# Kernel optimization log

Measured on AMD Instinct MI355X. Metric: run time of the kernel, lower is better.

Reference implementation:

```python
import jax, jax.numpy as jnp
import numpy as np

SCALE = 256 ** -0.5  # d_proj ** -0.5

def setup_inputs() -> dict:
    key = jax.random.key(0)
    k1, k2, k3, k4 = jax.random.split(key, 4)
    B, L, T = 8, 2048, 512
    Dh, Dg, Dp = 1024, 768, 256
    H = jax.random.normal(k1, (B, L, Dh), dtype=jnp.float32)
    G = jax.random.normal(k2, (B, T, Dg), dtype=jnp.float32)
    mask = jnp.zeros((B, L), dtype=jnp.int32)  # True/nonzero = masked OUT
    Wk = jax.random.normal(k3, (Dh, Dp), dtype=jnp.float32) * (Dh ** -0.5)
    Wq = jax.random.normal(k4, (Dg, Dp), dtype=jnp.float32) * (Dg ** -0.5)
    return {"H": H, "G": G, "mask": mask, "Wk": Wk, "Wq": Wq}

def reference(H, G, mask, Wk, Wq):
    # K: [B,L,Dp], Q: [B,T,Dp]
    K = jnp.einsum('bld,dp->blp', H, Wk)
    Q = jnp.einsum('btd,dp->btp', G, Wq)
    # logits over keys L: [B,T,L]
    logits = jnp.einsum('btp,blp->btl', Q, K) * SCALE
    logits = jnp.where(mask[:, None, :] != 0, -jnp.inf, logits)
    alpha = jax.nn.softmax(logits, axis=-1)  # online-softmax in torch == exact softmax
    Z = jnp.einsum('btl,bld->btd', alpha, H)  # [B,T,Dh]
    return Z
```

## Files before the change

kernel.cpp:

```cpp
#include <hip/hip_runtime.h>
#include <math.h>

#define BATCH 8
#define LKEYS 2048
#define TQ    512
#define DH    1024
#define DG    768
#define DP    256
#define SCALE 0.0625f

typedef short  short8  __attribute__((ext_vector_type(8)));
typedef float  floatx4 __attribute__((ext_vector_type(4)));
typedef unsigned short u16x4 __attribute__((ext_vector_type(4)));
typedef unsigned short u16x8 __attribute__((ext_vector_type(8)));

typedef unsigned int __attribute__((address_space(1))) as1_uint;
typedef unsigned int __attribute__((address_space(3))) as3_uint;

__device__ __forceinline__ unsigned short f2b(float f) {
    union { float f; unsigned int u; } v; v.f = f;
    unsigned int u = v.u;
    unsigned int r = u + 0x7fffu + ((u >> 16) & 1u);
    if ((u & 0x7f800000u) == 0x7f800000u) r = u;
    return (unsigned short)(r >> 16);
}

__device__ __forceinline__ void gload_lds16(const void* g, void* l) {
    __builtin_amdgcn_global_load_lds((const as1_uint*)g, (as3_uint*)l, 16, 0, 0);
}

__host__ __device__ constexpr int wcnt_vm(int vm) {
    return (vm & 15) | ((vm >> 4) << 14) | (7 << 4) | (15 << 8);
}

template<int BM, int BN, int OMODE, int SWZ>
__global__ __launch_bounds__(256) void gemm_bf16_p(
    const unsigned short* __restrict__ Ap, const unsigned short* __restrict__ Bp,
    const int* __restrict__ maskp, void* __restrict__ Cp,
    int K, int lda, int ldb, int ldc,
    long sA, long sB, long sC, long sM, float scale)
{
    constexpr int FM = BM / 32, FN = BN / 32;
    constexpr int AI = BM / 64, BI = BN / 64;
    constexpr int NL = AI + BI;

    __shared__ unsigned short As[4][BM * 32];
    __shared__ unsigned short Bs[4][BN * 32];

    int bx = blockIdx.x, by = blockIdx.y;
    if (SWZ) {
        const int gx = gridDim.x;
        const int nwg = gx * gridDim.y;
        const int f = by * gx + bx;
        const int nper = nwg >> 3;
        const int fl = (f & 7) * nper + (f >> 3);
        bx = fl % gx; by = fl / gx;
    }
    const int z    = blockIdx.z;
    const int tid  = threadIdx.x;
    const int lane = tid & 63;
    const int wid  = tid >> 6;
    const int wr   = wid >> 1, wc = wid & 1;
    const int lrow = lane & 15;
    const int g    = lane >> 4;

    const unsigned short* A = Ap + (long)z * sA + (long)(by * BM) * lda;
    const unsigned short* B = Bp + (long)z * sB + (long)(bx * BN) * ldb;
    const int srow = tid >> 2, sslot = tid & 3;

    const int nt = K / 32;
    floatx4 acc[FM][FN] = {};

    auto stage = [&](int t, int b) {
        const int k0 = t * 32;
        #pragma unroll
        for (int i = 0; i < AI; ++i)
            gload_lds16(A + (long)(srow + i * 64) * lda + k0 + sslot * 8,
                        (void*)&As[b][(i * 256 + tid) * 8]);
        #pragma unroll
        for (int i = 0; i < BI; ++i)
            gload_lds16(B + (long)(srow + i * 64) * ldb + k0 + sslot * 8,
                        (void*)&Bs[b][(i * 256 + tid) * 8]);
    };

    stage(0, 0);
    stage(1, 1);
    for (int t = 0; t < nt; ++t) {
        if (t + 2 < nt) {
            stage(t + 2, (t + 2) & 3);
            __builtin_amdgcn_s_waitcnt(wcnt_vm(2 * NL));
        } else if (t + 1 < nt) {
            __builtin_amdgcn_s_waitcnt(wcnt_vm(NL));
        } else {
            __builtin_amdgcn_s_waitcnt(wcnt_vm(0));
        }
        __builtin_amdgcn_s_barrier();
        __builtin_amdgcn_sched_barrier(0);

        const int b = t & 3;
        short8 a[FM], bf[FN];
        #pragma unroll
        for (int m = 0; m < FM; ++m)
            a[m] = *(const short8*)&As[b][(wr * (BM / 2) + m * 16 + lrow) * 32 + g * 8];
        #pragma unroll
        for (int n = 0; n < FN; ++n)
            bf[n] = *(const short8*)&Bs[b][(wc * (BN / 2) + n * 16 + lrow) * 32 + g * 8];
        __builtin_amdgcn_s_setprio(1);
        #pragma unroll
        for (int m = 0; m < FM; ++m)
            #pragma unroll
            for (int n = 0; n < FN; ++n)
                acc[m][n] = __builtin_amdgcn_mfma_f32_16x16x32_bf16(
                    a[m], bf[n], acc[m][n], 0, 0, 0);
        __builtin_amdgcn_s_setprio(0);
        __builtin_amdgcn_sched_barrier(0);
    }

    const int orow = by * BM + wr * (BM / 2);
    const int ocol = bx * BN + wc * (BN / 2);
    if (OMODE == 0) {
        float* C = (float*)Cp + (long)z * sC;
        #pragma unroll
        for (int m = 0; m < FM; ++m)
            #pragma unroll
            for (int n = 0; n < FN; ++n)
                #pragma unroll
                for (int r = 0; r < 4; ++r)
                    C[(long)(orow + m * 16 + 4 * g + r) * ldc + ocol + n * 16 + lrow]
                        = acc[m][n][r];
    } else if (OMODE == 1) {
        unsigned short* C = (unsigned short*)Cp + (long)z * sC;
        #pragma unroll
        for (int m = 0; m < FM; ++m)
            #pragma unroll
            for (int n = 0; n < FN; ++n)
                #pragma unroll
                for (int r = 0; r < 4; ++r)
                    C[(long)(orow + m * 16 + 4 * g + r) * ldc + ocol + n * 16 + lrow]
                        = f2b(acc[m][n][r]);
    } else {
        const int* mask = maskp + (long)z * sM;
        float* C = (float*)Cp + (long)z * sC;
        #pragma unroll
        for (int n = 0; n < FN; ++n) {
            int c = ocol + n * 16 + lrow;
            bool masked = (mask[c] != 0);
            #pragma unroll
            for (int m = 0; m < FM; ++m)
                #pragma unroll
                for (int r = 0; r < 4; ++r)
                    C[(long)(orow + m * 16 + 4 * g + r) * ldc + c]
                        = masked ? -INFINITY : acc[m][n][r] * scale;
        }
    }
}

template<int BM, int BN, int OMODE, int SWZ>
__global__ __launch_bounds__(256) void gemm_f32a(
    const float* __restrict__ Ap, const unsigned short* __restrict__ Bp,
    void* __restrict__ Cp, int K, int lda, int ldb, int ldc)
{
    constexpr int FM = BM / 32, FN = BN / 32;
    constexpr int AI = BM / 64, BI = BN / 64;

    __shared__ unsigned short As[2][BM * 32];
    __shared__ unsigned short Bs[2][BN * 32];

    int bx = blockIdx.x, by = blockIdx.y;
    if (SWZ) {
        const int gx = gridDim.x;
        const int nwg = gx * gridDim.y;
        const int f = by * gx + bx;
        const int nper = nwg >> 3;
        const int fl = (f & 7) * nper + (f >> 3);
        bx = fl % gx; by = fl / gx;
    }
    const int tid  = threadIdx.x;
    const int lane = tid & 63;
    const int wid  = tid >> 6;
    const int wr   = wid >> 1, wc = wid & 1;
    const int lrow = lane & 15;
    const int g    = lane >> 4;

    const float* A = Ap + (long)(by * BM) * lda;
    const unsigned short* B = Bp + (long)(bx * BN) * ldb;
    const int srow = tid >> 2, sslot = tid & 3;

    floatx4 acc[FM][FN] = {};
    const int nt = K / 32;
    int cur = 0;

    {
        float4 pa[AI][2];
        #pragma unroll
        for (int i = 0; i < AI; ++i) {
            const float* p = A + (long)(srow + i * 64) * lda + sslot * 8;
            pa[i][0] = *(const float4*)p;
            pa[i][1] = *(const float4*)(p + 4);
        }
        #pragma unroll
        for (int i = 0; i < BI; ++i)
            gload_lds16(B + (long)(srow + i * 64) * ldb + sslot * 8,
                        (void*)&Bs[0][(i * 256 + tid) * 8]);
        #pragma unroll
        for (int i = 0; i < AI; ++i) {
            u16x8 w;
            w[0] = f2b(pa[i][0].x); w[1] = f2b(pa[i][0].y);
            w[2] = f2b(pa[i][0].z); w[3] = f2b(pa[i][0].w);
            w[4] = f2b(pa[i][1].x); w[5] = f2b(pa[i][1].y);
            w[6] = f2b(pa[i][1].z); w[7] = f2b(pa[i][1].w);
            *(u16x8*)&As[0][(i * 256 + tid) * 8] = w;
        }
    }
    __syncthreads();

    for (int t = 0; t < nt; ++t) {
        float4 pa[AI][2];
        const bool pf = (t + 1 < nt);
        if (pf) {
            int k0 = (t + 1) * 32;
            #pragma unroll
            for (int i = 0; i < AI; ++i) {
                const float* p = A + (long)(srow + i * 64) * lda + k0 + sslot * 8;
                pa[i][0] = *(const float4*)p;
                pa[i][1] = *(const float4*)(p + 4);
            }
            #pragma unroll
            for (int i = 0; i < BI; ++i)
                gload_lds16(B + (long)(srow + i * 64) * ldb + k0 + sslot * 8,
                            (void*)&Bs[cur ^ 1][(i * 256 + tid) * 8]);
        }
        short8 a[FM], bf[FN];
        #pragma unroll
        for (int m = 0; m < FM; ++m)
            a[m] = *(const short8*)&As[cur][(wr * (BM / 2) + m * 16 + lrow) * 32 + g * 8];
        #pragma unroll
        for (int n = 0; n < FN; ++n)
            bf[n] = *(const short8*)&Bs[cur][(wc * (BN / 2) + n * 16 + lrow) * 32 + g * 8];
        #pragma unroll
        for (int m = 0; m < FM; ++m)
            #pragma unroll
            for (int n = 0; n < FN; ++n)
                acc[m][n] = __builtin_amdgcn_mfma_f32_16x16x32_bf16(
                    a[m], bf[n], acc[m][n], 0, 0, 0);
        if (pf) {
            #pragma unroll
            for (int i = 0; i < AI; ++i) {
                u16x8 w;
                w[0] = f2b(pa[i][0].x); w[1] = f2b(pa[i][0].y);
                w[2] = f2b(pa[i][0].z); w[3] = f2b(pa[i][0].w);
                w[4] = f2b(pa[i][1].x); w[5] = f2b(pa[i][1].y);
                w[6] = f2b(pa[i][1].z); w[7] = f2b(pa[i][1].w);
                *(u16x8*)&As[cur ^ 1][(i * 256 + tid) * 8] = w;
            }
        }
        __syncthreads();
        cur ^= 1;
    }

    const int orow = by * BM + wr * (BM / 2);
    const int ocol = bx * BN + wc * (BN / 2);
    if (OMODE == 1) {
        unsigned short* C = (unsigned short*)Cp;
        #pragma unroll
        for (int m = 0; m < FM; ++m)
            #pragma unroll
            for (int n = 0; n < FN; ++n)
                #pragma unroll
                for (int r = 0; r < 4; ++r)
                    C[(long)(orow + m * 16 + 4 * g + r) * ldc + ocol + n * 16 + lrow]
                        = f2b(acc[m][n][r]);
    } else {
        float* C = (float*)Cp;
        #pragma unroll
        for (int m = 0; m < FM; ++m)
            #pragma unroll
            for (int n = 0; n < FN; ++n)
                #pragma unroll
                for (int r = 0; r < 4; ++r)
                    C[(long)(orow + m * 16 + 4 * g + r) * ldc + ocol + n * 16 + lrow]
                        = acc[m][n][r];
    }
}

__global__ __launch_bounds__(256) void transpose_w(
    const float* __restrict__ W, unsigned short* __restrict__ WT, int D, int P)
{
    __shared__ float t[32][33];
    const int d0 = blockIdx.x * 32, p0 = blockIdx.y * 32;
    const int tx = threadIdx.x & 31, ty = threadIdx.x >> 5;
    #pragma unroll
    for (int j = 0; j < 4; ++j)
        t[ty + 8 * j][tx] = W[(long)(d0 + ty + 8 * j) * P + p0 + tx];
    __syncthreads();
    #pragma unroll
    for (int j = 0; j < 4; ++j)
        WT[(long)(p0 + ty + 8 * j) * D + d0 + tx] = f2b(t[tx][ty + 8 * j]);
}

__global__ __launch_bounds__(256) void prep_H(
    const float* __restrict__ H, unsigned short* __restrict__ Hb,
    unsigned short* __restrict__ HbT)
{
    __shared__ float tf[32][33];
    const int z = blockIdx.z;
    const int d0 = blockIdx.x * 32, l0 = blockIdx.y * 32;
    const float* Hz = H + (long)z * LKEYS * DH;
    unsigned short* Hbz = Hb + (long)z * LKEYS * DH;
    unsigned short* Tz = HbT + (long)z * DH * LKEYS;
    const int r = threadIdx.x >> 3, c = threadIdx.x & 7;
    float4 v = *(const float4*)&Hz[(long)(l0 + r) * DH + d0 + 4 * c];
    u16x4 w;
    w[0] = f2b(v.x); w[1] = f2b(v.y); w[2] = f2b(v.z); w[3] = f2b(v.w);
    *(u16x4*)&Hbz[(long)(l0 + r) * DH + d0 + 4 * c] = w;
    tf[r][4 * c + 0] = v.x; tf[r][4 * c + 1] = v.y;
    tf[r][4 * c + 2] = v.z; tf[r][4 * c + 3] = v.w;
    __syncthreads();
    u16x4 o;
    o[0] = f2b(tf[4 * c + 0][r]); o[1] = f2b(tf[4 * c + 1][r]);
    o[2] = f2b(tf[4 * c + 2][r]); o[3] = f2b(tf[4 * c + 3][r]);
    *(u16x4*)&Tz[(long)(d0 + r) * LKEYS + l0 + 4 * c] = o;
}

__global__ __launch_bounds__(256) void prep_HT(
    const float* __restrict__ H, unsigned short* __restrict__ HbT)
{
    __shared__ float tf[32][33];
    const int z = blockIdx.z;
    const int d0 = blockIdx.x * 32, l0 = blockIdx.y * 32;
    const float* Hz = H + (long)z * LKEYS * DH;
    unsigned short* Tz = HbT + (long)z * DH * LKEYS;
    const int r = threadIdx.x >> 3, c = threadIdx.x & 7;
    float4 v = *(const float4*)&Hz[(long)(l0 + r) * DH + d0 + 4 * c];
    tf[r][4 * c + 0] = v.x; tf[r][4 * c + 1] = v.y;
    tf[r][4 * c + 2] = v.z; tf[r][4 * c + 3] = v.w;
    __syncthreads();
    u16x4 o;
    o[0] = f2b(tf[4 * c + 0][r]); o[1] = f2b(tf[4 * c + 1][r]);
    o[2] = f2b(tf[4 * c + 2][r]); o[3] = f2b(tf[4 * c + 3][r]);
    *(u16x4*)&Tz[(long)(d0 + r) * LKEYS + l0 + 4 * c] = o;
}

__global__ __launch_bounds__(256) void prep_G(
    const float* __restrict__ G, unsigned short* __restrict__ Gb)
{
    long i = ((long)blockIdx.x * 256 + threadIdx.x) * 8;
    float4 a = *(const float4*)&G[i];
    float4 b = *(const float4*)&G[i + 4];
    u16x8 w;
    w[0] = f2b(a.x); w[1] = f2b(a.y); w[2] = f2b(a.z); w[3] = f2b(a.w);
    w[4] = f2b(b.x); w[5] = f2b(b.y); w[6] = f2b(b.z); w[7] = f2b(b.w);
    *(u16x8*)&Gb[i] = w;
}

__global__ __launch_bounds__(256) void softmax_kernel(
    const float* __restrict__ S, unsigned short* __restrict__ Ab)
{
    const float4* row4 = (const float4*)(S + (long)blockIdx.x * LKEYS);
    u16x4* out4 = (u16x4*)(Ab + (long)blockIdx.x * LKEYS);
    const int tid = threadIdx.x;
    __shared__ float red[4];

    float4 v0 = row4[tid], v1 = row4[tid + 256];
    float m = fmaxf(fmaxf(fmaxf(v0.x, v0.y), fmaxf(v0.z, v0.w)),
                    fmaxf(fmaxf(v1.x, v1.y), fmaxf(v1.z, v1.w)));
    #pragma unroll
    for (int off = 32; off > 0; off >>= 1) m = fmaxf(m, __shfl_xor(m, off));
    if ((tid & 63) == 0) red[tid >> 6] = m;
    __syncthreads();
    m = fmaxf(fmaxf(red[0], red[1]), fmaxf(red[2], red[3]));

    float e[8];
    e[0] = __expf(v0.x - m); e[1] = __expf(v0.y - m);
    e[2] = __expf(v0.z - m); e[3] = __expf(v0.w - m);
    e[4] = __expf(v1.x - m); e[5] = __expf(v1.y - m);
    e[6] = __expf(v1.z - m); e[7] = __expf(v1.w - m);
    float s = ((e[0] + e[1]) + (e[2] + e[3])) + ((e[4] + e[5]) + (e[6] + e[7]));
    #pragma unroll
    for (int off = 32; off > 0; off >>= 1) s += __shfl_xor(s, off);
    __syncthreads();
    if ((tid & 63) == 0) red[tid >> 6] = s;
    __syncthreads();
    s = red[0] + red[1] + red[2] + red[3];

    float inv = 1.0f / s;
    u16x4 a0, a1;
    a0[0] = f2b(e[0] * inv); a0[1] = f2b(e[1] * inv);
    a0[2] = f2b(e[2] * inv); a0[3] = f2b(e[3] * inv);
    a1[0] = f2b(e[4] * inv); a1[1] = f2b(e[5] * inv);
    a1[2] = f2b(e[6] * inv); a1[3] = f2b(e[7] * inv);
    out4[tid] = a0; out4[tid + 256] = a1;
}

extern "C" void kernel_launch(void* const* d_in, const int* in_sizes, int n_in,
                              void* d_out, int out_size, void* d_ws, size_t ws_size,
                              hipStream_t stream)
{
    const float* H    = (const float*)d_in[0];
    const float* G    = (const float*)d_in[1];
    const int*   mask = (const int*)  d_in[2];
    const float* Wk   = (const float*)d_in[3];
    const float* Wq   = (const float*)d_in[4];
    float*       Z    = (float*)d_out;

    unsigned short* WkT = (unsigned short*)d_ws;
    unsigned short* WqT = WkT + 262144;
    unsigned short* Ab  = WqT + 196608;

    transpose_w<<<dim3(DH / 32, DP / 32), 256, 0, stream>>>(Wk, WkT, DH, DP);
    transpose_w<<<dim3(DG / 32, DP / 32), 256, 0, stream>>>(Wq, WqT, DG, DP);

    const size_t NEED_A = 101580800ull;

    if (ws_size >= NEED_A) {
        unsigned short* Kb  = Ab  + 8388608;
        unsigned short* Qb  = Kb  + 4194304;
        unsigned short* Gb  = Qb  + 1048576;
        unsigned short* HbT = Gb  + 3145728;
        unsigned short* Hb  = HbT + 16777216;
        float*          S   = (float*)Hb;

        prep_G<<<1536, 256, 0, stream>>>(G, Gb);
        prep_H<<<dim3(DH / 32, LKEYS / 32, BATCH), 256, 0, stream>>>(H, Hb, HbT);

        gemm_bf16_p<128, 64, 1, 1><<<dim3(4, 128, 1), 256, 0, stream>>>(
            Hb, WkT, nullptr, Kb, DH, DH, DH, DP, 0, 0, 0, 0, 1.f);

        gemm_bf16_p<64, 64, 1, 1><<<dim3(4, 64, 1), 256, 0, stream>>>(
            Gb, WqT, nullptr, Qb, DG, DG, DG, DP, 0, 0, 0, 0, 1.f);

        gemm_bf16_p<128, 64, 2, 0><<<dim3(32, 4, BATCH), 256, 0, stream>>>(
            Qb, Kb, mask, S, DP, DP, DP, LKEYS,
            (long)TQ * DP, (long)LKEYS * DP, (long)TQ * LKEYS, (long)LKEYS, SCALE);

        softmax_kernel<<<BATCH * TQ, 256, 0, stream>>>(S, Ab);

        gemm_bf16_p<128, 64, 0, 1><<<dim3(16, 4, BATCH), 256, 0, stream>>>(
            Ab, HbT, nullptr, Z, LKEYS, LKEYS, LKEYS, DH,
            (long)TQ * LKEYS, (long)DH * LKEYS, (long)TQ * DH, 0, 1.f);
    } else {
        unsigned short* R   = Ab + 8388608;
        unsigned short* Kb  = R;
        unsigned short* Qb  = Kb + 4194304;
        float*          S   = (float*)(Qb + 1048576);
        unsigned short* HbT = R;

        gemm_f32a<128, 64, 1, 1><<<dim3(4, 128, 1), 256, 0, stream>>>(
            H, WkT, Kb, DH, DH, DH, DP);
        gemm_f32a<64, 64, 1, 1><<<dim3(4, 64, 1), 256, 0, stream>>>(
            G, WqT, Qb, DG, DG, DG, DP);

        gemm_bf16_p<128, 64, 2, 0><<<dim3(32, 4, BATCH), 256, 0, stream>>>(
            Qb, Kb, mask, S, DP, DP, DP, LKEYS,
            (long)TQ * DP, (long)LKEYS * DP, (long)TQ * LKEYS, (long)LKEYS, SCALE);

        softmax_kernel<<<BATCH * TQ, 256, 0, stream>>>(S, Ab);

        prep_HT<<<dim3(DH / 32, LKEYS / 32, BATCH), 256, 0, stream>>>(H, HbT);

        gemm_bf16_p<128, 64, 0, 1><<<dim3(16, 4, BATCH), 256, 0, stream>>>(
            Ab, HbT, nullptr, Z, LKEYS, LKEYS, LKEYS, DH,
            (long)TQ * LKEYS, (long)DH * LKEYS, (long)TQ * DH, 0, 1.f);
    }
}
```

Baseline: 126.4 us.

## Split-K the final attention GEMM, deepen LDS prefetch, drop fallback path

The final alpha·H GEMM is split along the key dimension into two halves. This doubles the grid from 512 to 1024 workgroups, and a reduce_add kernel then sums the two fp32 partial outputs into Z. The GEMM pipeline now prefetches three stages ahead instead of two, with each stage issued after the barrier. The QK^T logits GEMM now uses block swizzling, the low-workspace fallback path is removed, and the vmcnt encoding drops its high bits. The split costs an extra 32 MB partial-output write plus a read-back and an extra kernel launch, and it assumes the workspace is always large enough.

```diff
diff --git a/kernel.cpp b/kernel.cpp
--- a/kernel.cpp
+++ b/kernel.cpp
@@ -30,15 +30,15 @@
 }
 
 __host__ __device__ constexpr int wcnt_vm(int vm) {
-    return (vm & 15) | ((vm >> 4) << 14) | (7 << 4) | (15 << 8);
-}
-
-template<int BM, int BN, int OMODE, int SWZ>
+    return (vm & 15) | (7 << 4) | (15 << 8);
+}
+
+template<int BM, int BN, int OMODE, int SWZ, int KSPLIT>
 __global__ __launch_bounds__(256) void gemm_bf16_p(
     const unsigned short* __restrict__ Ap, const unsigned short* __restrict__ Bp,
     const int* __restrict__ maskp, void* __restrict__ Cp,
     int K, int lda, int ldb, int ldc,
-    long sA, long sB, long sC, long sM, float scale)
+    long sA, long sB, long sC, long sM, long sP, float scale)
 {
     constexpr int FM = BM / 32, FN = BN / 32;
     constexpr int AI = BM / 64, BI = BN / 64;
@@ -56,7 +56,11 @@
         const int fl = (f & 7) * nper + (f >> 3);
         bx = fl % gx; by = fl / gx;
     }
-    const int z    = blockIdx.z;
+    const int zz   = blockIdx.z;
+    const int z    = (KSPLIT == 2) ? (zz & 7) : zz;
+    const int half = (KSPLIT == 2) ? (zz >> 3) : 0;
+    const int koff = half * K;
+
     const int tid  = threadIdx.x;
     const int lane = tid & 63;
     const int wid  = tid >> 6;
@@ -64,8 +68,8 @@
     const int lrow = lane & 15;
     const int g    = lane >> 4;
 
-    const unsigned short* A = Ap + (long)z * sA + (long)(by * BM) * lda;
-    const unsigned short* B = Bp + (long)z * sB + (long)(bx * BN) * ldb;
+    const unsigned short* A = Ap + (long)z * sA + (long)(by * BM) * lda + koff;
+    const unsigned short* B = Bp + (long)z * sB + (long)(bx * BN) * ldb + koff;
     const int srow = tid >> 2, sslot = tid & 3;
 
     const int nt = K / 32;
@@ -85,16 +89,14 @@
 
     stage(0, 0);
     stage(1, 1);
+    stage(2, 2);
     for (int t = 0; t < nt; ++t) {
-        if (t + 2 < nt) {
-            stage(t + 2, (t + 2) & 3);
-            __builtin_amdgcn_s_waitcnt(wcnt_vm(2 * NL));
-        } else if (t + 1 < nt) {
-            __builtin_amdgcn_s_waitcnt(wcnt_vm(NL));
-        } else {
-            __builtin_amdgcn_s_waitcnt(wcnt_vm(0));
-        }
+        if (t < nt - 2)      __builtin_amdgcn_s_waitcnt(wcnt_vm(2 * NL));
+        else if (t == nt - 2) __builtin_amdgcn_s_waitcnt(wcnt_vm(NL));
+        else                  __builtin_amdgcn_s_waitcnt(wcnt_vm(0));
         __builtin_amdgcn_s_barrier();
+        __builtin_amdgcn_sched_barrier(0);
+        if (t + 3 < nt) stage(t + 3, (t + 3) & 3);
         __builtin_amdgcn_sched_barrier(0);
 
         const int b = t & 3;
@@ -119,7 +121,7 @@
     const int orow = by * BM + wr * (BM / 2);
     const int ocol = bx * BN + wc * (BN / 2);
     if (OMODE == 0) {
-        float* C = (float*)Cp + (long)z * sC;
+        float* C = (float*)Cp + (long)z * sC + (long)half * sP;
         #pragma unroll
         for (int m = 0; m < FM; ++m)
             #pragma unroll
@@ -155,132 +157,13 @@
     }
 }
 
-template<int BM, int BN, int OMODE, int SWZ>
-__global__ __launch_bounds__(256) void gemm_f32a(
-    const float* __restrict__ Ap, const unsigned short* __restrict__ Bp,
-    void* __restrict__ Cp, int K, int lda, int ldb, int ldc)
-{
-    constexpr int FM = BM / 32, FN = BN / 32;
-    constexpr int AI = BM / 64, BI = BN / 64;
-
-    __shared__ unsigned short As[2][BM * 32];
-    __shared__ unsigned short Bs[2][BN * 32];
-
-    int bx = blockIdx.x, by = blockIdx.y;
-    if (SWZ) {
-        const int gx = gridDim.x;
-        const int nwg = gx * gridDim.y;
-        const int f = by * gx + bx;
-        const int nper = nwg >> 3;
-        const int fl = (f & 7) * nper + (f >> 3);
-        bx = fl % gx; by = fl / gx;
-    }
-    const int tid  = threadIdx.x;
-    const int lane = tid & 63;
-    const int wid  = tid >> 6;
-    const int wr   = wid >> 1, wc = wid & 1;
-    const int lrow = lane & 15;
-    const int g    = lane >> 4;
-
-    const float* A = Ap + (long)(by * BM) * lda;
-    const unsigned short* B = Bp + (long)(bx * BN) * ldb;
-    const int srow = tid >> 2, sslot = tid & 3;
-
-    floatx4 acc[FM][FN] = {};
-    const int nt = K / 32;
-    int cur = 0;
-
-    {
-        float4 pa[AI][2];
-        #pragma unroll
-        for (int i = 0; i < AI; ++i) {
-            const float* p = A + (long)(srow + i * 64) * lda + sslot * 8;
-            pa[i][0] = *(const float4*)p;
-            pa[i][1] = *(const float4*)(p + 4);
-        }
-        #pragma unroll
-        for (int i = 0; i < BI; ++i)
-            gload_lds16(B + (long)(srow + i * 64) * ldb + sslot * 8,
-                        (void*)&Bs[0][(i * 256 + tid) * 8]);
-        #pragma unroll
-        for (int i = 0; i < AI; ++i) {
-            u16x8 w;
-            w[0] = f2b(pa[i][0].x); w[1] = f2b(pa[i][0].y);
-            w[2] = f2b(pa[i][0].z); w[3] = f2b(pa[i][0].w);
-            w[4] = f2b(pa[i][1].x); w[5] = f2b(pa[i][1].y);
-            w[6] = f2b(pa[i][1].z); w[7] = f2b(pa[i][1].w);
-            *(u16x8*)&As[0][(i * 256 + tid) * 8] = w;
-        }
-    }
-    __syncthreads();
-
-    for (int t = 0; t < nt; ++t) {
-        float4 pa[AI][2];
-        const bool pf = (t + 1 < nt);
-        if (pf) {
-            int k0 = (t + 1) * 32;
-            #pragma unroll
-            for (int i = 0; i < AI; ++i) {
-                const float* p = A + (long)(srow + i * 64) * lda + k0 + sslot * 8;
-                pa[i][0] = *(const float4*)p;
-                pa[i][1] = *(const float4*)(p + 4);
-            }
-            #pragma unroll
-            for (int i = 0; i < BI; ++i)
-                gload_lds16(B + (long)(srow + i * 64) * ldb + k0 + sslot * 8,
-                            (void*)&Bs[cur ^ 1][(i * 256 + tid) * 8]);
-        }
-        short8 a[FM], bf[FN];
-        #pragma unroll
-        for (int m = 0; m < FM; ++m)
-            a[m] = *(const short8*)&As[cur][(wr * (BM / 2) + m * 16 + lrow) * 32 + g * 8];
-        #pragma unroll
-        for (int n = 0; n < FN; ++n)
-            bf[n] = *(const short8*)&Bs[cur][(wc * (BN / 2) + n * 16 + lrow) * 32 + g * 8];
-        #pragma unroll
-        for (int m = 0; m < FM; ++m)
-            #pragma unroll
-            for (int n = 0; n < FN; ++n)
-                acc[m][n] = __builtin_amdgcn_mfma_f32_16x16x32_bf16(
-                    a[m], bf[n], acc[m][n], 0, 0, 0);
-        if (pf) {
-            #pragma unroll
-            for (int i = 0; i < AI; ++i) {
-                u16x8 w;
-                w[0] = f2b(pa[i][0].x); w[1] = f2b(pa[i][0].y);
-                w[2] = f2b(pa[i][0].z); w[3] = f2b(pa[i][0].w);
-                w[4] = f2b(pa[i][1].x); w[5] = f2b(pa[i][1].y);
-                w[6] = f2b(pa[i][1].z); w[7] = f2b(pa[i][1].w);
-                *(u16x8*)&As[cur ^ 1][(i * 256 + tid) * 8] = w;
-            }
-        }
-        __syncthreads();
-        cur ^= 1;
-    }
-
-    const int orow = by * BM + wr * (BM / 2);
-    const int ocol = bx * BN + wc * (BN / 2);
-    if (OMODE == 1) {
-        unsigned short* C = (unsigned short*)Cp;
-        #pragma unroll
-        for (int m = 0; m < FM; ++m)
-            #pragma unroll
-            for (int n = 0; n < FN; ++n)
-                #pragma unroll
-                for (int r = 0; r < 4; ++r)
-                    C[(long)(orow + m * 16 + 4 * g + r) * ldc + ocol + n * 16 + lrow]
-                        = f2b(acc[m][n][r]);
-    } else {
-        float* C = (float*)Cp;
-        #pragma unroll
-        for (int m = 0; m < FM; ++m)
-            #pragma unroll
-            for (int n = 0; n < FN; ++n)
-                #pragma unroll
-                for (int r = 0; r < 4; ++r)
-                    C[(long)(orow + m * 16 + 4 * g + r) * ldc + ocol + n * 16 + lrow]
-                        = acc[m][n][r];
-    }
+__global__ __launch_bounds__(256) void reduce_add(
+    const float4* __restrict__ P0, const float4* __restrict__ P1,
+    float4* __restrict__ Zo)
+{
+    long i = (long)blockIdx.x * 256 + threadIdx.x;
+    float4 a = P0[i], b = P1[i];
+    Zo[i] = make_float4(a.x + b.x, a.y + b.y, a.z + b.z, a.w + b.w);
 }
 
 __global__ __launch_bounds__(256) void transpose_w(
@@ -322,25 +205,6 @@
     *(u16x4*)&Tz[(long)(d0 + r) * LKEYS + l0 + 4 * c] = o;
 }
 
-__global__ __launch_bounds__(256) void prep_HT(
-    const float* __restrict__ H, unsigned short* __restrict__ HbT)
-{
-    __shared__ float tf[32][33];
-    const int z = blockIdx.z;
-    const int d0 = blockIdx.x * 32, l0 = blockIdx.y * 32;
-    const float* Hz = H + (long)z * LKEYS * DH;
-    unsigned short* Tz = HbT + (long)z * DH * LKEYS;
-    const int r = threadIdx.x >> 3, c = threadIdx.x & 7;
-    float4 v = *(const float4*)&Hz[(long)(l0 + r) * DH + d0 + 4 * c];
-    tf[r][4 * c + 0] = v.x; tf[r][4 * c + 1] = v.y;
-    tf[r][4 * c + 2] = v.z; tf[r][4 * c + 3] = v.w;
-    __syncthreads();
-    u16x4 o;
-    o[0] = f2b(tf[4 * c + 0][r]); o[1] = f2b(tf[4 * c + 1][r]);
-    o[2] = f2b(tf[4 * c + 2][r]); o[3] = f2b(tf[4 * c + 3][r]);
-    *(u16x4*)&Tz[(long)(d0 + r) * LKEYS + l0 + 4 * c] = o;
-}
-
 __global__ __launch_bounds__(256) void prep_G(
     const float* __restrict__ G, unsigned short* __restrict__ Gb)
 {
@@ -406,60 +270,38 @@
     unsigned short* WkT = (unsigned short*)d_ws;
     unsigned short* WqT = WkT + 262144;
     unsigned short* Ab  = WqT + 196608;
+    unsigned short* Kb  = Ab  + 8388608;
+    unsigned short* Qb  = Kb  + 4194304;
+    unsigned short* Gb  = Qb  + 1048576;
+    unsigned short* HbT = Gb  + 3145728;
+    unsigned short* Hb  = HbT + 16777216;
+    float*          S   = (float*)Hb;
+    float*          Zp  = (float*)Hb;
 
     transpose_w<<<dim3(DH / 32, DP / 32), 256, 0, stream>>>(Wk, WkT, DH, DP);
     transpose_w<<<dim3(DG / 32, DP / 32), 256, 0, stream>>>(Wq, WqT, DG, DP);
 
-    const size_t NEED_A = 101580800ull;
-
-    if (ws_size >= NEED_A) {
-        unsigned short* Kb  = Ab  + 8388608;
-        unsigned short* Qb  = Kb  + 4194304;
-        unsigned short* Gb  = Qb  + 1048576;
-        unsigned short* HbT = Gb  + 3145728;
-        unsigned short* Hb  = HbT + 16777216;
-        float*          S   = (float*)Hb;
-
-        prep_G<<<1536, 256, 0, stream>>>(G, Gb);
-        prep_H<<<dim3(DH / 32, LKEYS / 32, BATCH), 256, 0, stream>>>(H, Hb, HbT);
-
-        gemm_bf16_p<128, 64, 1, 1><<<dim3(4, 128, 1), 256, 0, stream>>>(
-            Hb, WkT, nullptr, Kb, DH, DH, DH, DP, 0, 0, 0, 0, 1.f);
-
-        gemm_bf16_p<64, 64, 1, 1><<<dim3(4, 64, 1), 256, 0, stream>>>(
-            Gb, WqT, nullptr, Qb, DG, DG, DG, DP, 0, 0, 0, 0, 1.f);
-
-        gemm_bf16_p<128, 64, 2, 0><<<dim3(32, 4, BATCH), 256, 0, stream>>>(
-            Qb, Kb, mask, S, DP, DP, DP, LKEYS,
-            (long)TQ * DP, (long)LKEYS * DP, (long)TQ * LKEYS, (long)LKEYS, SCALE);
-
-        softmax_kernel<<<BATCH * TQ, 256, 0, stream>>>(S, Ab);
-
-        gemm_bf16_p<128, 64, 0, 1><<<dim3(16, 4, BATCH), 256, 0, stream>>>(
-            Ab, HbT, nullptr, Z, LKEYS, LKEYS, LKEYS, DH,
-            (long)TQ * LKEYS, (long)DH * LKEYS, (long)TQ * DH, 0, 1.f);
-    } else {
-        unsigned short* R   = Ab + 8388608;
-        unsigned short* Kb  = R;
-        unsigned short* Qb  = Kb + 4194304;
-        float*          S   = (float*)(Qb + 1048576);
-        unsigned short* HbT = R;
-
-        gemm_f32a<128, 64, 1, 1><<<dim3(4, 128, 1), 256, 0, stream>>>(
-            H, WkT, Kb, DH, DH, DH, DP);
-        gemm_f32a<64, 64, 1, 1><<<dim3(4, 64, 1), 256, 0, stream>>>(
-            G, WqT, Qb, DG, DG, DG, DP);
-
-        gemm_bf16_p<128, 64, 2, 0><<<dim3(32, 4, BATCH), 256, 0, stream>>>(
-            Qb, Kb, mask, S, DP, DP, DP, LKEYS,
-            (long)TQ * DP, (long)LKEYS * DP, (long)TQ * LKEYS, (long)LKEYS, SCALE);
-
-        softmax_kernel<<<BATCH * TQ, 256, 0, stream>>>(S, Ab);
-
-        prep_HT<<<dim3(DH / 32, LKEYS / 32, BATCH), 256, 0, stream>>>(H, HbT);
-
-        gemm_bf16_p<128, 64, 0, 1><<<dim3(16, 4, BATCH), 256, 0, stream>>>(
-            Ab, HbT, nullptr, Z, LKEYS, LKEYS, LKEYS, DH,
-            (long)TQ * LKEYS, (long)DH * LKEYS, (long)TQ * DH, 0, 1.f);
-    }
-}
+    prep_G<<<1536, 256, 0, stream>>>(G, Gb);
+    prep_H<<<dim3(DH / 32, LKEYS / 32, BATCH), 256, 0, stream>>>(H, Hb, HbT);
+
+    gemm_bf16_p<128, 64, 1, 1, 1><<<dim3(4, 128, 1), 256, 0, stream>>>(
+        Hb, WkT, nullptr, Kb, DH, DH, DH, DP, 0, 0, 0, 0, 0, 1.f);
+
+    gemm_bf16_p<64, 64, 1, 1, 1><<<dim3(4, 64, 1), 256, 0, stream>>>(
+        Gb, WqT, nullptr, Qb, DG, DG, DG, DP, 0, 0, 0, 0, 0, 1.f);
+
+    gemm_bf16_p<128, 64, 2, 1, 1><<<dim3(32, 4, BATCH), 256, 0, stream>>>(
+        Qb, Kb, mask, S, DP, DP, DP, LKEYS,
+        (long)TQ * DP, (long)LKEYS * DP, (long)TQ * LKEYS, (long)LKEYS, 0, SCALE);
+
+    softmax_kernel<<<BATCH * TQ, 256, 0, stream>>>(S, Ab);
+
+    gemm_bf16_p<128, 64, 0, 1, 2><<<dim3(16, 4, 2 * BATCH), 256, 0, stream>>>(
+        Ab, HbT, nullptr, Zp, LKEYS / 2, LKEYS, LKEYS, DH,
+        (long)TQ * LKEYS, (long)DH * LKEYS, (long)TQ * DH, 0,
+        (long)BATCH * TQ * DH, 1.f);
+
+    reduce_add<<<(BATCH * TQ * DH / 4) / 256, 256, 0, stream>>>(
+        (const float4*)Zp, (const float4*)(Zp + (long)BATCH * TQ * DH),
+        (float4*)Z);
+}
```

Measured after the change: 144.8 us. 14.6% more time.
